# Kernel optimization log

Hardware: AMD Instinct MI355X
Metric: run time of the kernel (lower is better)

## Reference

```python
import jax, jax.numpy as jnp
import numpy as np

B = 256
NO_A, NF_A = 64, 4   # class A: n_obj, n_field (all state fields)
NO_B, NF_B = 32, 3   # class B
NS = NF_A + NF_B     # total state fields = 7
DIN, DL, DG, DH = 128, 64, 64, 256
DGE = DG * NF_A + DG * NF_B          # 448 global encoding dim
DIN_A = DGE + DL * NF_A              # 704 decoder input dim, class A
DIN_B = DGE + DL * NF_B              # 640 decoder input dim, class B
NP = 2  # distribution params per field (mean, scale)


def lrelu(x):
    return jnp.where(x >= 0, x, 0.01 * x)


def setup_inputs() -> dict:
    key = jax.random.key(0)
    ks = iter(jax.random.split(key, 40))
    def rn(shape, s=1.0):
        return jax.random.normal(next(ks), shape, jnp.float32) * s
    def w(shape):
        return rn(shape, 0.05)
    def rb(shape):
        return jax.random.randint(next(ks), shape, 0, 2).astype(bool)
    inp = dict(
        x_A=rn((B, NO_A, NF_A, DIN)),
        x_B=rn((B, NO_B, NF_B, DIN)),
        global_mask=rb((B, NS, NF_A + NF_B)),
        local_mask_A=rb((B, NF_A, NF_A)),
        local_mask_B=rb((B, NF_B, NF_B)),
        objmask_A=rb((B, NO_A)),
        objmask_B=rb((B, NO_B)),
        enc_Wl_A=w((DIN, DL)), enc_bl_A=w((DL,)),
        enc_Wg_A=w((DIN, DG)), enc_bg_A=w((DG,)),
        enc_Wl_B=w((DIN, DL)), enc_bl_B=w((DL,)),
        enc_Wg_B=w((DIN, DG)), enc_bg_B=w((DG,)),
        dec_W1_A=w((NF_A, DIN_A, DH)), dec_b1_A=w((NF_A, DH)),
        dec_W2_A=w((NF_A, DH, DH)), dec_b2_A=w((NF_A, DH)),
        dec_Wp_A=w((NF_A, DH, NP)), dec_bp_A=w((NF_A, NP)),
        dec_W1_B=w((NF_B, DIN_B, DH)), dec_b1_B=w((NF_B, DH)),
        dec_W2_B=w((NF_B, DH, DH)), dec_b2_B=w((NF_B, DH)),
        dec_Wp_B=w((NF_B, DH, NP)), dec_bp_B=w((NF_B, NP)),
        rw_W1=w((DGE, DH)), rw_b1=w((DH,)),
        rw_W2=w((DH, DH)), rw_b2=w((DH,)),
        rw_W3=w((DH, 1)), rw_b3=w((1,)),
    )
    return inp


def encode_local(x, Wl, bl, attrmask):
    # x: (B, O, F, DIN) -> (B, O, S, F*DL), masked_retain over attrmask (B, S, F)
    h = jax.nn.relu(x @ Wl + bl)                                  # (B,O,F,DL)
    y = jnp.where(attrmask[:, None, :, :, None], h[:, :, None, :, :], 0.0)  # (B,O,S,F,DL)
    return y.reshape(y.shape[0], y.shape[1], y.shape[2], -1)


def encode_global(x, Wg, bg, attrmask, objmask):
    # x: (B, O, F, DIN), attrmask: (B, NS, F), objmask: (B, O)
    h = x @ Wg + bg                                               # (B,O,F,DG)
    h = jnp.where(objmask[:, :, None, None], h, 0.0)
    r = jax.nn.relu(jnp.sum(h, axis=1))                           # (B,F,DG) sum-pool over objects
    y = jnp.where(attrmask[:, :, :, None], r[:, None], 0.0)       # (B,NS,F,DG)
    y = jnp.concatenate([y, r[:, None]], axis=1)                  # (B,NS+1,F,DG)
    return y.reshape(y.shape[0], y.shape[1], -1)


def decode(x, W1, b1, W2, b2, Wp, bp):
    # x: (B, O, S, Din); per-field (s) decoders stacked on leading axis
    h = lrelu(jnp.einsum('bosi,sid->bosd', x, W1) + b1)
    h = lrelu(jnp.einsum('bosd,sde->bose', h, W2) + b2)
    return jnp.einsum('bose,sep->bosp', h, Wp) + bp               # (B,O,S,NP)


def reference(x_A, x_B, global_mask, local_mask_A, local_mask_B, objmask_A, objmask_B,
              enc_Wl_A, enc_bl_A, enc_Wg_A, enc_bg_A,
              enc_Wl_B, enc_bl_B, enc_Wg_B, enc_bg_B,
              dec_W1_A, dec_b1_A, dec_W2_A, dec_b2_A, dec_Wp_A, dec_bp_A,
              dec_W1_B, dec_b1_B, dec_W2_B, dec_b2_B, dec_Wp_B, dec_bp_B,
              rw_W1, rw_b1, rw_W2, rw_b2, rw_W3, rw_b3):
    g_A = encode_global(x_A, enc_Wg_A, enc_bg_A, global_mask[:, :, :NF_A], objmask_A)
    g_B = encode_global(x_B, enc_Wg_B, enc_bg_B, global_mask[:, :, NF_A:], objmask_B)
    G = jnp.concatenate([g_A, g_B], axis=2)                       # (B, NS+1, DGE)

    l_A = encode_local(x_A, enc_Wl_A, enc_bl_A, local_mask_A)     # (B,NO_A,NF_A,NF_A*DL)
    gs_A = jnp.broadcast_to(G[:, None, :NF_A, :], (B, NO_A, NF_A, DGE))
    out_A = decode(jnp.concatenate([l_A, gs_A], axis=3),
                   dec_W1_A, dec_b1_A, dec_W2_A, dec_b2_A, dec_Wp_A, dec_bp_A)

    l_B = encode_local(x_B, enc_Wl_B, enc_bl_B, local_mask_B)
    gs_B = jnp.broadcast_to(G[:, None, NF_A:NS, :], (B, NO_B, NF_B, DGE))
    out_B = decode(jnp.concatenate([l_B, gs_B], axis=3),
                   dec_W1_B, dec_b1_B, dec_W2_B, dec_b2_B, dec_Wp_B, dec_bp_B)

    h = lrelu(G[:, -1, :] @ rw_W1 + rw_b1)
    h = lrelu(h @ rw_W2 + rw_b2)
    reward = (h @ rw_W3 + rw_b3)[:, 0]                            # (B,)
    return out_A, out_B, reward
```

## Files before the change

### kernel.cpp

```cpp
#include <hip/hip_runtime.h>
#include <hip/hip_bf16.h>

constexpr int Bn   = 256;
constexpr int NOA  = 64, NFA = 4;
constexpr int NOB  = 32, NFB = 3;
constexpr int NS   = 7;
constexpr int DIN  = 128, DL = 64, DG = 64, DH = 256;
constexpr int DGE  = 448;
constexpr int DINA = 704;
constexpr int DINB = 640;

typedef short  short8v __attribute__((ext_vector_type(8)));
typedef float  f32x4   __attribute__((ext_vector_type(4)));

__device__ __forceinline__ unsigned short f2bf(float x) {
  union { float f; unsigned int u; } a; a.f = x;
  unsigned int r = a.u + 0x7fff + ((a.u >> 16) & 1);
  return (unsigned short)(r >> 16);
}


struct MidArgs {
  const float *xA, *xB, *WlA, *WlB, *blA, *blB;
  unsigned short *hlA, *hlB;
  const int *omA, *omB;
  const float *WgA, *bgA, *WgB, *bgB;
  float *rA, *rB;
  const float *W1A, *W1B, *W2A, *W2B;
  unsigned short *W1tA, *W1tB, *W1gtA, *W1gtB, *W2tA, *W2tB;
};

template<int F>
__device__ void hl_body(const float* __restrict__ x, const float* __restrict__ Wl,
                        const float* __restrict__ bl, unsigned short* __restrict__ hlf,
                        int m0, unsigned char* smem) {
  auto Asb = reinterpret_cast<unsigned short(*)[72]>(smem);
  auto Bsb = reinterpret_cast<unsigned short(*)[136]>(smem + 36864);
  float (*tile)[65] = reinterpret_cast<float(*)[65]>(smem);
  const int t = threadIdx.x, w = t >> 6, lane = t & 63;
  const int lr = lane & 15, lg = lane >> 4;
  constexpr int KB1 = 2 * F;

#pragma unroll
  for (int i = 0; i < 32; ++i) {
    int idx = t + i * 256;
    tile[idx >> 6][idx & 63] = Wl[idx];
  }
  __syncthreads();
#pragma unroll
  for (int i = 0; i < 32; ++i) {
    int idx = t + i * 256;
    int n = idx >> 7, k = idx & 127;
    Bsb[n][k] = f2bf(tile[k][n]);
  }
  __syncthreads();

  f32x4 acc[4][4] = {};
  for (int k0 = 0; k0 < DIN; k0 += 64) {
    const float* xp = x + (size_t)(m0 + t) * DIN + k0;
#pragma unroll
    for (int j = 0; j < 8; ++j) {
      float4 a = *(const float4*)(xp + j * 8);
      float4 b = *(const float4*)(xp + j * 8 + 4);
      union { short8v v; unsigned short e[8]; } u;
      u.e[0] = f2bf(a.x); u.e[1] = f2bf(a.y); u.e[2] = f2bf(a.z); u.e[3] = f2bf(a.w);
      u.e[4] = f2bf(b.x); u.e[5] = f2bf(b.y); u.e[6] = f2bf(b.z); u.e[7] = f2bf(b.w);
      *reinterpret_cast<short8v*>(&Asb[t][j * 8]) = u.v;
    }
#pragma unroll
    for (int ks = 0; ks < 2; ++ks) {
      short8v af[4], bf[4];
#pragma unroll
      for (int mi = 0; mi < 4; ++mi)
        af[mi] = *reinterpret_cast<const short8v*>(&Asb[w * 64 + mi * 16 + lr][ks * 32 + lg * 8]);
#pragma unroll
      for (int ni = 0; ni < 4; ++ni)
        bf[ni] = *reinterpret_cast<const short8v*>(&Bsb[ni * 16 + lr][k0 + ks * 32 + lg * 8]);
#pragma unroll
      for (int mi = 0; mi < 4; ++mi)
#pragma unroll
        for (int ni = 0; ni < 4; ++ni)
          acc[mi][ni] = __builtin_amdgcn_mfma_f32_16x16x32_bf16(
              af[mi], bf[ni], acc[mi][ni], 0, 0, 0);
    }
  }
#pragma unroll
  for (int mi = 0; mi < 4; ++mi)
#pragma unroll
    for (int ni = 0; ni < 4; ++ni)
#pragma unroll
      for (int reg = 0; reg < 4; ++reg) {
        int row = mi * 16 + lg * 4 + reg;
        int col = ni * 16 + lr;
        float v = fmaxf(acc[mi][ni][reg] + bl[col], 0.f);
        Asb[w * 64 + row][col] = f2bf(v);
      }
  const int mpb = m0 + w * 64;
#pragma unroll
  for (int j = 0; j < 8; ++j) {
    int c = lane + j * 64;
    int ml = c >> 3, dls = c & 7;
    int mp = mpb + ml;
    int mrow = mp / F, f = mp % F;
    int m6 = mrow >> 6, mi = (mrow >> 4) & 3, lr2 = mrow & 15;
    int kb = 2 * f + (dls >> 2), lg2 = dls & 3;
    size_t dst = ((((size_t)m6 * KB1 + kb) * 4 + mi) * 64 + (lg2 * 16 + lr2)) * 8;
    *reinterpret_cast<short8v*>(hlf + dst) =
        *reinterpret_cast<const short8v*>(&Asb[w * 64 + ml][dls * 8]);
  }
}

template<int O, int F>
__device__ void xsum_rg_body(const float* __restrict__ x, const int* __restrict__ om,
                             const float* __restrict__ Wg, const float* __restrict__ bg,
                             float* __restrict__ r, int b, unsigned char* smem) {
  float* xsm = reinterpret_cast<float*>(smem + 36864 + 17408);
  const int t = threadIdx.x, f = t >> 6, lane = t & 63;
  if (f >= F) return;
  unsigned long long bal = __ballot(lane < O && om[(size_t)b * O + lane] != 0);
  float cnt = (float)__popcll(bal);
  float a0 = 0.f, a1 = 0.f;
  const float* xb = x + ((size_t)b * O * F + f) * DIN + lane;
#pragma unroll 8
  for (int o = 0; o < O; ++o) {
    float m = (float)((bal >> o) & 1ull);
    a0 += m * xb[(size_t)o * F * DIN];
    a1 += m * xb[(size_t)o * F * DIN + 64];
  }
  xsm[f * 128 + lane] = a0;
  xsm[f * 128 + lane + 64] = a1;
  asm volatile("s_waitcnt lgkmcnt(0)" ::: "memory");
  float acc = 0.f;
  const float* wp = Wg + lane;
#pragma unroll 8
  for (int i = 0; i < DIN; ++i) acc += xsm[f * 128 + i] * wp[(size_t)i * DG];
  acc += cnt * bg[lane];
  r[((size_t)b * F + f) * DG + lane] = fmaxf(acc, 0.f);
}

__device__ void wtrans_tile(const float* __restrict__ src, unsigned short* __restrict__ dst,
                            int N, int DINc, int koff, int Kout,
                            int s, int kt, int nt, unsigned char* smem) {
  float (*tile)[65] = reinterpret_cast<float(*)[65]>(smem);
  const int t = threadIdx.x;
#pragma unroll
  for (int i = 0; i < 16; ++i) {
    int rr = (t >> 6) + i * 4, c = t & 63;
    tile[rr][c] = src[((size_t)s * DINc + koff + kt * 64 + rr) * N + nt * 64 + c];
  }
  __syncthreads();
#pragma unroll
  for (int i = 0; i < 2; ++i) {
    int cidx = t + i * 256;
    int n = cidx >> 3, kc = (cidx & 7) * 8;
    union { short8v v; unsigned short e[8]; } u;
#pragma unroll
    for (int j = 0; j < 8; ++j) u.e[j] = f2bf(tile[kc + j][n]);
    *reinterpret_cast<short8v*>(dst + ((size_t)s * N + nt * 64 + n) * Kout + kt * 64 + kc) = u.v;
  }
}

__device__ void wtrans_frag(const float* __restrict__ src, unsigned short* __restrict__ dst,
                            int DINc, int koff, int KB,
                            int s, int kt, int nt, unsigned char* smem) {
  float (*tile)[65] = reinterpret_cast<float(*)[65]>(smem);
  const int t = threadIdx.x;
#pragma unroll
  for (int i = 0; i < 16; ++i) {
    int rr = (t >> 6) + i * 4, c = t & 63;
    tile[rr][c] = src[((size_t)s * DINc + koff + kt * 64 + rr) * 256 + nt * 64 + c];
  }
  __syncthreads();
#pragma unroll
  for (int i = 0; i < 2; ++i) {
    int cidx = t + i * 256;
    int nl = cidx >> 3, kslot = cidx & 7;
    union { short8v v; unsigned short e[8]; } u;
#pragma unroll
    for (int j = 0; j < 8; ++j) u.e[j] = f2bf(tile[kslot * 8 + j][nl]);
    int kb = kt * 2 + (kslot >> 2);
    int lane = (kslot & 3) * 16 + (nl & 15);
    int nchunk = nt * 4 + (nl >> 4);
    *reinterpret_cast<short8v*>(
        dst + ((((size_t)s * KB + kb) * 16 + nchunk) * 64 + lane) * 8) = u.v;
  }
}

__global__ __launch_bounds__(256) void mid_kernel(MidArgs a) {
  __shared__ __align__(16) unsigned char smem[56320];
  const int bid = blockIdx.x;
  if (bid < 256) {
    hl_body<NFA>(a.xA, a.WlA, a.blA, a.hlA, bid * 256, smem);
    xsum_rg_body<NOA, NFA>(a.xA, a.omA, a.WgA, a.bgA, a.rA, bid, smem);
  } else if (bid < 352) {
    hl_body<NFB>(a.xB, a.WlB, a.blB, a.hlB, (bid - 256) * 256, smem);
  } else if (bid < 608) {
    xsum_rg_body<NOB, NFB>(a.xB, a.omB, a.WgB, a.bgB, a.rB, bid - 352, smem);
  } else {
    int r = bid - 608;
    if (r < 64)       { wtrans_frag(a.W1A, a.W1tA, DINA, 0, 8,
                                    r / 16, (r % 16) >> 2, r & 3, smem); }
    else if (r < 100) { r -= 64;  wtrans_frag(a.W1B, a.W1tB, DINB, 0, 6,
                                    r / 12, (r % 12) >> 2, r & 3, smem); }
    else if (r < 212) { r -= 100; wtrans_tile(a.W1A, a.W1gtA, 256, DINA, NFA * DL, DGE,
                                    r / 28, (r % 28) >> 2, r & 3, smem); }
    else if (r < 296) { r -= 212; wtrans_tile(a.W1B, a.W1gtB, 256, DINB, NFB * DL, DGE,
                                    r / 28, (r % 28) >> 2, r & 3, smem); }
    else if (r < 360) { r -= 296; wtrans_frag(a.W2A, a.W2tA, DH, 0, 8,
                                    r / 16, (r % 16) >> 2, r & 3, smem); }
    else              { r -= 360; wtrans_frag(a.W2B, a.W2tB, DH, 0, 8,
                                    r / 16, (r % 16) >> 2, r & 3, smem); }
  }
}

struct GprArgs {
  const float *rA, *rB; const int *gm;
  const unsigned short *W1gtA, *W1gtB;
  const float *b1A, *b1B;
  float *g1A, *g1B;
  const float *rwW1, *rwb1, *rwW2, *rwb2, *rwW3, *rwb3;
  float *outR;
  const unsigned short *hlA, *hlB;
};

__device__ void warm_body(const unsigned short* __restrict__ p, int n16) {
  const int4* q = reinterpret_cast<const int4*>(p);
  const int t = threadIdx.x;
  for (int i = 0; i < n16; ++i) {
    int4 v = q[t + i * 256];
    asm volatile("" :: "v"(v.x), "v"(v.y), "v"(v.z), "v"(v.w));
  }
}

__device__ void gpart_body(const GprArgs& a, int bx, int sg, unsigned char* smem) {
  auto Asb = reinterpret_cast<unsigned short(*)[72]>(smem);
  auto Bsb = reinterpret_cast<unsigned short(*)[72]>(smem + 9216);
  const int t = threadIdx.x, w = t >> 6, lane = t & 63;
  const int lr = lane & 15, lg = lane >> 4;
  const int m0 = bx * 64;
  const unsigned short* W1gt; const float* b1; float* g1; int S, sl;
  if (sg < NFA) { W1gt = a.W1gtA; b1 = a.b1A; g1 = a.g1A; S = NFA; sl = sg; }
  else          { W1gt = a.W1gtB; b1 = a.b1B; g1 = a.g1B; S = NFB; sl = sg - NFA; }

  f32x4 acc[4][4] = {};
  for (int kt = 0; kt < 7; ++kt) {
    __syncthreads();
    const int f = kt;
    const float* rsrc = (f < NFA) ? (a.rA + (size_t)f * DG) : (a.rB + (size_t)(f - NFA) * DG);
    const int rstride = (f < NFA) ? NFA * DG : NFB * DG;
#pragma unroll
    for (int i = 0; i < 2; ++i) {
      int c = t + i * 256;
      int row = c >> 3, kc = (c & 7) * 8;
      int b = m0 + row;
      float mk = (a.gm[((size_t)b * NS + sg) * NS + f] != 0) ? 1.f : 0.f;
      const float* rp = rsrc + (size_t)b * rstride + kc;
      union { short8v v; unsigned short e[8]; } u;
#pragma unroll
      for (int j = 0; j < 8; ++j) u.e[j] = f2bf(mk * rp[j]);
      *reinterpret_cast<short8v*>(&Asb[row][kc]) = u.v;
    }
#pragma unroll
    for (int i = 0; i < 8; ++i) {
      int c = t + i * 256;
      int n = c >> 3, kc = (c & 7) * 8;
      *reinterpret_cast<short8v*>(&Bsb[n][kc]) = *reinterpret_cast<const short8v*>(
          W1gt + ((size_t)sl * 256 + n) * DGE + kt * 64 + kc);
    }
    __syncthreads();
#pragma unroll
    for (int ks = 0; ks < 2; ++ks) {
      short8v af[4], bf[4];
#pragma unroll
      for (int mi = 0; mi < 4; ++mi)
        af[mi] = *reinterpret_cast<const short8v*>(&Asb[mi * 16 + lr][ks * 32 + lg * 8]);
#pragma unroll
      for (int ni = 0; ni < 4; ++ni)
        bf[ni] = *reinterpret_cast<const short8v*>(&Bsb[w * 64 + ni * 16 + lr][ks * 32 + lg * 8]);
#pragma unroll
      for (int mi = 0; mi < 4; ++mi)
#pragma unroll
        for (int ni = 0; ni < 4; ++ni)
          acc[mi][ni] = __builtin_amdgcn_mfma_f32_16x16x32_bf16(
              af[mi], bf[ni], acc[mi][ni], 0, 0, 0);
    }
  }
#pragma unroll
  for (int mi = 0; mi < 4; ++mi)
#pragma unroll
    for (int reg = 0; reg < 4; ++reg) {
      int b = m0 + mi * 16 + lg * 4 + reg;
#pragma unroll
      for (int ni = 0; ni < 4; ++ni) {
        int col = w * 64 + ni * 16 + lr;
        g1[((size_t)b * S + sl) * DH + col] = acc[mi][ni][reg] + b1[(size_t)sl * DH + col];
      }
    }
}

__device__ void reward_body(const GprArgs& a, int b, unsigned char* smem) {
  float* Gs = reinterpret_cast<float*>(smem);
  float* h1 = Gs + DGE;
  float* red = h1 + DH;
  const int t = threadIdx.x;
  for (int j = t; j < DGE; j += 256)
    Gs[j] = (j < NFA * DG) ? a.rA[((size_t)b * NFA + (j >> 6)) * DG + (j & 63)]
                           : a.rB[((size_t)b * NFB + ((j - NFA * DG) >> 6)) * DG + (j & 63)];
  __syncthreads();
  float acc = a.rwb1[t];
  for (int j = 0; j < DGE; ++j) acc += Gs[j] * a.rwW1[(size_t)j * DH + t];
  h1[t] = (acc >= 0.f) ? acc : 0.01f * acc;
  __syncthreads();
  acc = a.rwb2[t];
  for (int j = 0; j < DH; ++j) acc += h1[j] * a.rwW2[(size_t)j * DH + t];
  acc = (acc >= 0.f) ? acc : 0.01f * acc;
  red[t] = acc * a.rwW3[t];
  __syncthreads();
  for (int off = 128; off > 0; off >>= 1) {
    if (t < off) red[t] += red[t + off];
    __syncthreads();
  }
  if (t == 0) a.outR[b] = red[0] + a.rwb3[0];
}

__global__ __launch_bounds__(256) void gpr_kernel(GprArgs a) {
  __shared__ __align__(16) unsigned char smem[46080];
  const int bid = blockIdx.x;
  if (bid < 256) {
    int xcd = bid & 7, idx = bid >> 3;
    int m6 = (idx >> 1) * 16 + xcd * 2 + (idx & 1);
    warm_body(a.hlA + (size_t)m6 * 16384, 8);
  } else if (bid < 384) {
    int local = bid - 256;
    int xcd = local & 7, idx = local >> 3;
    int m6 = (idx >> 1) * 16 + xcd * 2 + (idx & 1);
    warm_body(a.hlB + (size_t)m6 * 12288, 6);
  } else if (bid < 412) {
    gpart_body(a, (bid - 384) & 3, (bid - 384) >> 2, smem);
  } else {
    reward_body(a, bid - 412, smem);
  }
}

struct DecArgs {
  const unsigned short *hlA, *hlB, *W1tA, *W1tB, *W2tA, *W2tB;
  const int *lmA, *lmB;
  const float *g1A, *g1B, *WpA, *WpB, *b2A, *b2B, *bpA, *bpB;
  float *outA, *outB;
};

template<int NO, int F>
__device__ __forceinline__ void dec_body(
    int mt, int s, unsigned short* h1s , float* red ,
    const unsigned short* __restrict__ hlf, const int* __restrict__ lm,
    const float* __restrict__ g1,
    const unsigned short* __restrict__ W1f, const unsigned short* __restrict__ W2f,
    const float* __restrict__ Wp, const float* __restrict__ b2,
    const float* __restrict__ bp, float* __restrict__ out) {
  constexpr int KB1 = 2 * F;
  const int t = threadIdx.x, w = t >> 6, lane = t & 63;
  const int lr = lane & 15, lg = lane >> 4;
  const int mh = w >> 2, nq = w & 3;
  const int m6 = mt * 2 + mh;
  const int m0 = mt * 128;

  unsigned mkl = 0, mkh = 0;
#pragma unroll
  for (int f = 0; f < F; ++f) {
    if (NO == 64) {
      unsigned bit = (lm[((size_t)m6 * F + s) * F + f] != 0) ? 1u : 0u;
      mkl |= bit << f; mkh |= bit << f;
    } else {
      int b0 = m6 * 2;
      if (lm[((size_t)b0 * F + s) * F + f])       mkl |= 1u << f;
      if (lm[((size_t)(b0 + 1) * F + s) * F + f]) mkh |= 1u << f;
    }
  }
  float g1r[2][4];
#pragma unroll
  for (int ni = 0; ni < 4; ++ni) {
    int col = nq * 64 + ni * 16 + lr;
    if (NO == 64) {
      g1r[0][ni] = g1[((size_t)m6 * F + s) * DH + col];
      g1r[1][ni] = g1r[0][ni];
    } else {
      g1r[0][ni] = g1[((size_t)(m6 * 2) * F + s) * DH + col];
      g1r[1][ni] = g1[((size_t)(m6 * 2 + 1) * F + s) * DH + col];
    }
  }

  f32x4 acc[4][4] = {};
  const short8v zero8 = {0, 0, 0, 0, 0, 0, 0, 0};

  const unsigned short* Afb = hlf + (size_t)m6 * KB1 * 2048 + lane * 8;
  const unsigned short* B1b = W1f + ((size_t)s * KB1 * 16 + nq * 4) * 512 + lane * 8;
#pragma unroll
  for (int kb = 0; kb < KB1; ++kb) {
    const int f = kb >> 1;
    short8v af[4], bf[4];
#pragma unroll
    for (int mi = 0; mi < 4; ++mi)
      af[mi] = *reinterpret_cast<const short8v*>(Afb + (size_t)kb * 2048 + mi * 512);
    const bool bl = (mkl >> f) & 1, bh = (mkh >> f) & 1;
#pragma unroll
    for (int mi = 0; mi < 4; ++mi) {
      const bool ok = (mi < 2) ? bl : bh;
      af[mi] = ok ? af[mi] : zero8;
    }
#pragma unroll
    for (int ni = 0; ni < 4; ++ni)
      bf[ni] = *reinterpret_cast<const short8v*>(B1b + (size_t)kb * 8192 + ni * 512);
#pragma unroll
    for (int mi = 0; mi < 4; ++mi)
#pragma unroll
      for (int ni = 0; ni < 4; ++ni)
        acc[mi][ni] = __builtin_amdgcn_mfma_f32_16x16x32_bf16(
            af[mi], bf[ni], acc[mi][ni], 0, 0, 0);
  }

#pragma unroll
  for (int mi = 0; mi < 4; ++mi) {
    int gi = (NO == 32) ? (mi >> 1) : 0;
#pragma unroll
    for (int reg = 0; reg < 4; ++reg) {
      int row = mh * 64 + mi * 16 + lg * 4 + reg;
#pragma unroll
      for (int ni = 0; ni < 4; ++ni) {
        int col = nq * 64 + ni * 16 + lr;
        float v = acc[mi][ni][reg] + g1r[gi][ni];
        v = (v >= 0.f) ? v : 0.01f * v;
        h1s[row * 264 + col] = f2bf(v);
        acc[mi][ni][reg] = 0.f;
      }
    }
  }
  __syncthreads();

  const unsigned short* B2b = W2f + ((size_t)s * 8 * 16 + nq * 4) * 512 + lane * 8;
#pragma unroll
  for (int kb = 0; kb < 8; ++kb) {
    short8v af[4], bf[4];
#pragma unroll
    for (int mi = 0; mi < 4; ++mi)
      af[mi] = *reinterpret_cast<const short8v*>(
          h1s + (mh * 64 + mi * 16 + lr) * 264 + kb * 32 + lg * 8);
#pragma unroll
    for (int ni = 0; ni < 4; ++ni)
      bf[ni] = *reinterpret_cast<const short8v*>(B2b + (size_t)kb * 8192 + ni * 512);
#pragma unroll
    for (int mi = 0; mi < 4; ++mi)
#pragma unroll
      for (int ni = 0; ni < 4; ++ni)
        acc[mi][ni] = __builtin_amdgcn_mfma_f32_16x16x32_bf16(
            af[mi], bf[ni], acc[mi][ni], 0, 0, 0);
  }

  float part[4][4][2] = {};
  const float* Wps = Wp + (size_t)s * DH * 2;
  const float* b2s = b2 + (size_t)s * DH;
#pragma unroll
  for (int ni = 0; ni < 4; ++ni) {
    int col = nq * 64 + ni * 16 + lr;
    float wp0 = Wps[col * 2 + 0], wp1 = Wps[col * 2 + 1], bb2 = b2s[col];
#pragma unroll
    for (int mi = 0; mi < 4; ++mi)
#pragma unroll
      for (int reg = 0; reg < 4; ++reg) {
        float v = acc[mi][ni][reg] + bb2;
        v = (v >= 0.f) ? v : 0.01f * v;
        part[mi][reg][0] += v * wp0;
        part[mi][reg][1] += v * wp1;
      }
  }
#pragma unroll
  for (int off = 1; off < 16; off <<= 1)
#pragma unroll
    for (int mi = 0; mi < 4; ++mi)
#pragma unroll
      for (int reg = 0; reg < 4; ++reg) {
        part[mi][reg][0] += __shfl_xor(part[mi][reg][0], off, 64);
        part[mi][reg][1] += __shfl_xor(part[mi][reg][1], off, 64);
      }
  if (lr == 0)
#pragma unroll
    for (int mi = 0; mi < 4; ++mi)
#pragma unroll
      for (int reg = 0; reg < 4; ++reg) {
        int rowin = mi * 16 + lg * 4 + reg;
        red[((size_t)w * 64 + rowin) * 2 + 0] = part[mi][reg][0];
        red[((size_t)w * 64 + rowin) * 2 + 1] = part[mi][reg][1];
      }
  __syncthreads();
  if (t < 256) {
    int row = t >> 1, p = t & 1;
    int mhr = row >> 6, rowin = row & 63;
    float sum = 0.f;
#pragma unroll
    for (int q = 0; q < 4; ++q)
      sum += red[((size_t)(mhr * 4 + q) * 64 + rowin) * 2 + p];
    out[((size_t)(m0 + row) * F + s) * 2 + p] = sum + bp[(size_t)s * 2 + p];
  }
}

__global__ __launch_bounds__(512, 4) void dec_kernel(DecArgs a) {
  __shared__ __align__(16) unsigned short h1s[128 * 264];
  __shared__ float red[1024];
  const int bid = blockIdx.x;
  if (bid < 512) {
    dec_body<NOA, NFA>(bid & 127, bid >> 7, h1s, red, a.hlA, a.lmA, a.g1A,
                       a.W1tA, a.W2tA, a.WpA, a.b2A, a.bpA, a.outA);
  } else {
    int r = bid - 512;
    dec_body<NOB, NFB>(r & 63, r >> 6, h1s, red, a.hlB, a.lmB, a.g1B,
                       a.W1tB, a.W2tB, a.WpB, a.b2B, a.bpB, a.outB);
  }
}

extern "C" void kernel_launch(void* const* d_in, const int* in_sizes, int n_in,
                              void* d_out, int out_size, void* d_ws, size_t ws_size,
                              hipStream_t stream) {
  const float* x_A  = (const float*)d_in[0];
  const float* x_B  = (const float*)d_in[1];
  const int*   gm   = (const int*)d_in[2];
  const int*   lmA  = (const int*)d_in[3];
  const int*   lmB  = (const int*)d_in[4];
  const int*   omA  = (const int*)d_in[5];
  const int*   omB  = (const int*)d_in[6];
  const float* Wl_A = (const float*)d_in[7];
  const float* bl_A = (const float*)d_in[8];
  const float* Wg_A = (const float*)d_in[9];
  const float* bg_A = (const float*)d_in[10];
  const float* Wl_B = (const float*)d_in[11];
  const float* bl_B = (const float*)d_in[12];
  const float* Wg_B = (const float*)d_in[13];
  const float* bg_B = (const float*)d_in[14];
  const float* W1_A = (const float*)d_in[15];
  const float* b1_A = (const float*)d_in[16];
  const float* W2_A = (const float*)d_in[17];
  const float* b2_A = (const float*)d_in[18];
  const float* Wp_A = (const float*)d_in[19];
  const float* bp_A = (const float*)d_in[20];
  const float* W1_B = (const float*)d_in[21];
  const float* b1_B = (const float*)d_in[22];
  const float* W2_B = (const float*)d_in[23];
  const float* b2_B = (const float*)d_in[24];
  const float* Wp_B = (const float*)d_in[25];
  const float* bp_B = (const float*)d_in[26];
  const float* rwW1 = (const float*)d_in[27];
  const float* rwb1 = (const float*)d_in[28];
  const float* rwW2 = (const float*)d_in[29];
  const float* rwb2 = (const float*)d_in[30];
  const float* rwW3 = (const float*)d_in[31];
  const float* rwb3 = (const float*)d_in[32];

  float* ws   = (float*)d_ws;
  float* rA   = ws;
  float* rB   = rA + 65536;
  float* g1A  = rB + 49152;
  float* g1B  = g1A + 262144;
  unsigned short* us    = (unsigned short*)(g1B + 196608);
  unsigned short* hlA   = us;
  unsigned short* hlB   = hlA + 4194304;
  unsigned short* W1tA  = hlB + 1572864;
  unsigned short* W1tB  = W1tA + 262144;
  unsigned short* W2tA  = W1tB + 147456;
  unsigned short* W2tB  = W2tA + 262144;
  unsigned short* W1gtA = W2tB + 196608;
  unsigned short* W1gtB = W1gtA + 458752;

  float* outA = (float*)d_out;
  float* outB = outA + 131072;
  float* outR = outA + 180224;

  MidArgs m;
  m.xA = x_A; m.xB = x_B; m.WlA = Wl_A; m.WlB = Wl_B; m.blA = bl_A; m.blB = bl_B;
  m.hlA = hlA; m.hlB = hlB; m.omA = omA; m.omB = omB;
  m.WgA = Wg_A; m.bgA = bg_A; m.WgB = Wg_B; m.bgB = bg_B;
  m.rA = rA; m.rB = rB;
  m.W1A = W1_A; m.W1B = W1_B; m.W2A = W2_A; m.W2B = W2_B;
  m.W1tA = W1tA; m.W1tB = W1tB; m.W1gtA = W1gtA; m.W1gtB = W1gtB;
  m.W2tA = W2tA; m.W2tB = W2tB;

  GprArgs g;
  g.rA = rA; g.rB = rB; g.gm = gm; g.W1gtA = W1gtA; g.W1gtB = W1gtB;
  g.b1A = b1_A; g.b1B = b1_B; g.g1A = g1A; g.g1B = g1B;
  g.rwW1 = rwW1; g.rwb1 = rwb1; g.rwW2 = rwW2; g.rwb2 = rwb2;
  g.rwW3 = rwW3; g.rwb3 = rwb3; g.outR = outR;
  g.hlA = hlA; g.hlB = hlB;

  DecArgs d;
  d.hlA = hlA; d.hlB = hlB; d.W1tA = W1tA; d.W1tB = W1tB;
  d.W2tA = W2tA; d.W2tB = W2tB; d.lmA = lmA; d.lmB = lmB;
  d.g1A = g1A; d.g1B = g1B; d.WpA = Wp_A; d.WpB = Wp_B;
  d.b2A = b2_A; d.b2B = b2_B; d.bpA = bp_A; d.bpB = bp_B;
  d.outA = outA; d.outB = outB;

  mid_kernel<<<1016, 256, 0, stream>>>(m);
  gpr_kernel<<<668, 256, 0, stream>>>(g);
  dec_kernel<<<704, 512, 0, stream>>>(d);
}
```

Before: 94.42 us.

## Fuse local encoder into decoder kernel, keeping hl activations in LDS

The local-encoder GEMM (x @ Wl, relu) now runs inside the decoder kernel. Each block computes its 64-row hl tile straight into shared memory and loops over all state fields s, instead of writing hl to global memory and reading it back. The cache-warming blocks and the global hl buffer are removed, and Wl is pre-packed into MFMA fragment layout in the first kernel. The trade-off is fewer, larger decoder blocks: 384 blocks of 256 threads replace 704 of 512, each doing F sequential passes, which lowers parallelism and occupancy.

```diff
diff --git a/kernel.cpp b/kernel.cpp
--- a/kernel.cpp
+++ b/kernel.cpp
@@ -20,101 +20,20 @@
 }
 
 
-struct MidArgs {
-  const float *xA, *xB, *WlA, *WlB, *blA, *blB;
-  unsigned short *hlA, *hlB;
+struct Pre1Args {
+  const float *xA, *xB;
   const int *omA, *omB;
   const float *WgA, *bgA, *WgB, *bgB;
   float *rA, *rB;
-  const float *W1A, *W1B, *W2A, *W2B;
-  unsigned short *W1tA, *W1tB, *W1gtA, *W1gtB, *W2tA, *W2tB;
+  const float *WlA, *WlB, *W1A, *W1B, *W2A, *W2B;
+  unsigned short *WlFA, *WlFB, *W1tA, *W1tB, *W1gtA, *W1gtB, *W2tA, *W2tB;
 };
-
-template<int F>
-__device__ void hl_body(const float* __restrict__ x, const float* __restrict__ Wl,
-                        const float* __restrict__ bl, unsigned short* __restrict__ hlf,
-                        int m0, unsigned char* smem) {
-  auto Asb = reinterpret_cast<unsigned short(*)[72]>(smem);
-  auto Bsb = reinterpret_cast<unsigned short(*)[136]>(smem + 36864);
-  float (*tile)[65] = reinterpret_cast<float(*)[65]>(smem);
-  const int t = threadIdx.x, w = t >> 6, lane = t & 63;
-  const int lr = lane & 15, lg = lane >> 4;
-  constexpr int KB1 = 2 * F;
-
-#pragma unroll
-  for (int i = 0; i < 32; ++i) {
-    int idx = t + i * 256;
-    tile[idx >> 6][idx & 63] = Wl[idx];
-  }
-  __syncthreads();
-#pragma unroll
-  for (int i = 0; i < 32; ++i) {
-    int idx = t + i * 256;
-    int n = idx >> 7, k = idx & 127;
-    Bsb[n][k] = f2bf(tile[k][n]);
-  }
-  __syncthreads();
-
-  f32x4 acc[4][4] = {};
-  for (int k0 = 0; k0 < DIN; k0 += 64) {
-    const float* xp = x + (size_t)(m0 + t) * DIN + k0;
-#pragma unroll
-    for (int j = 0; j < 8; ++j) {
-      float4 a = *(const float4*)(xp + j * 8);
-      float4 b = *(const float4*)(xp + j * 8 + 4);
-      union { short8v v; unsigned short e[8]; } u;
-      u.e[0] = f2bf(a.x); u.e[1] = f2bf(a.y); u.e[2] = f2bf(a.z); u.e[3] = f2bf(a.w);
-      u.e[4] = f2bf(b.x); u.e[5] = f2bf(b.y); u.e[6] = f2bf(b.z); u.e[7] = f2bf(b.w);
-      *reinterpret_cast<short8v*>(&Asb[t][j * 8]) = u.v;
-    }
-#pragma unroll
-    for (int ks = 0; ks < 2; ++ks) {
-      short8v af[4], bf[4];
-#pragma unroll
-      for (int mi = 0; mi < 4; ++mi)
-        af[mi] = *reinterpret_cast<const short8v*>(&Asb[w * 64 + mi * 16 + lr][ks * 32 + lg * 8]);
-#pragma unroll
-      for (int ni = 0; ni < 4; ++ni)
-        bf[ni] = *reinterpret_cast<const short8v*>(&Bsb[ni * 16 + lr][k0 + ks * 32 + lg * 8]);
-#pragma unroll
-      for (int mi = 0; mi < 4; ++mi)
-#pragma unroll
-        for (int ni = 0; ni < 4; ++ni)
-          acc[mi][ni] = __builtin_amdgcn_mfma_f32_16x16x32_bf16(
-              af[mi], bf[ni], acc[mi][ni], 0, 0, 0);
-    }
-  }
-#pragma unroll
-  for (int mi = 0; mi < 4; ++mi)
-#pragma unroll
-    for (int ni = 0; ni < 4; ++ni)
-#pragma unroll
-      for (int reg = 0; reg < 4; ++reg) {
-        int row = mi * 16 + lg * 4 + reg;
-        int col = ni * 16 + lr;
-        float v = fmaxf(acc[mi][ni][reg] + bl[col], 0.f);
-        Asb[w * 64 + row][col] = f2bf(v);
-      }
-  const int mpb = m0 + w * 64;
-#pragma unroll
-  for (int j = 0; j < 8; ++j) {
-    int c = lane + j * 64;
-    int ml = c >> 3, dls = c & 7;
-    int mp = mpb + ml;
-    int mrow = mp / F, f = mp % F;
-    int m6 = mrow >> 6, mi = (mrow >> 4) & 3, lr2 = mrow & 15;
-    int kb = 2 * f + (dls >> 2), lg2 = dls & 3;
-    size_t dst = ((((size_t)m6 * KB1 + kb) * 4 + mi) * 64 + (lg2 * 16 + lr2)) * 8;
-    *reinterpret_cast<short8v*>(hlf + dst) =
-        *reinterpret_cast<const short8v*>(&Asb[w * 64 + ml][dls * 8]);
-  }
-}
 
 template<int O, int F>
 __device__ void xsum_rg_body(const float* __restrict__ x, const int* __restrict__ om,
                              const float* __restrict__ Wg, const float* __restrict__ bg,
-                             float* __restrict__ r, int b, unsigned char* smem) {
-  float* xsm = reinterpret_cast<float*>(smem + 36864 + 17408);
+                             float* __restrict__ r, int b, float* smem) {
+  float* xsm = smem;
   const int t = threadIdx.x, f = t >> 6, lane = t & 63;
   if (f >= F) return;
   unsigned long long bal = __ballot(lane < O && om[(size_t)b * O + lane] != 0);
@@ -140,7 +59,7 @@
 
 __device__ void wtrans_tile(const float* __restrict__ src, unsigned short* __restrict__ dst,
                             int N, int DINc, int koff, int Kout,
-                            int s, int kt, int nt, unsigned char* smem) {
+                            int s, int kt, int nt, float* smem) {
   float (*tile)[65] = reinterpret_cast<float(*)[65]>(smem);
   const int t = threadIdx.x;
 #pragma unroll
@@ -162,7 +81,7 @@
 
 __device__ void wtrans_frag(const float* __restrict__ src, unsigned short* __restrict__ dst,
                             int DINc, int koff, int KB,
-                            int s, int kt, int nt, unsigned char* smem) {
+                            int s, int kt, int nt, float* smem) {
   float (*tile)[65] = reinterpret_cast<float(*)[65]>(smem);
   const int t = threadIdx.x;
 #pragma unroll
@@ -186,53 +105,66 @@
   }
 }
 
-__global__ __launch_bounds__(256) void mid_kernel(MidArgs a) {
-  __shared__ __align__(16) unsigned char smem[56320];
+__device__ void wl_frag(const float* __restrict__ src, unsigned short* __restrict__ dst,
+                        int kt, float* smem) {
+  float (*tile)[65] = reinterpret_cast<float(*)[65]>(smem);
+  const int t = threadIdx.x;
+#pragma unroll
+  for (int i = 0; i < 16; ++i) {
+    int rr = (t >> 6) + i * 4, c = t & 63;
+    tile[rr][c] = src[(size_t)(kt * 64 + rr) * 64 + c];
+  }
+  __syncthreads();
+#pragma unroll
+  for (int i = 0; i < 2; ++i) {
+    int cidx = t + i * 256;
+    int nl = cidx >> 3, kslot = cidx & 7;
+    union { short8v v; unsigned short e[8]; } u;
+#pragma unroll
+    for (int j = 0; j < 8; ++j) u.e[j] = f2bf(tile[kslot * 8 + j][nl]);
+    int kb = kt * 2 + (kslot >> 2);
+    int lane = (kslot & 3) * 16 + (nl & 15);
+    int nchunk = nl >> 4;
+    *reinterpret_cast<short8v*>(dst + (((size_t)kb * 4 + nchunk) * 64 + lane) * 8) = u.v;
+  }
+}
+
+__global__ __launch_bounds__(256) void pre1_kernel(Pre1Args a) {
+  __shared__ __align__(16) float smem[64 * 65];
   const int bid = blockIdx.x;
   if (bid < 256) {
-    hl_body<NFA>(a.xA, a.WlA, a.blA, a.hlA, bid * 256, smem);
     xsum_rg_body<NOA, NFA>(a.xA, a.omA, a.WgA, a.bgA, a.rA, bid, smem);
-  } else if (bid < 352) {
-    hl_body<NFB>(a.xB, a.WlB, a.blB, a.hlB, (bid - 256) * 256, smem);
-  } else if (bid < 608) {
-    xsum_rg_body<NOB, NFB>(a.xB, a.omB, a.WgB, a.bgB, a.rB, bid - 352, smem);
+  } else if (bid < 512) {
+    xsum_rg_body<NOB, NFB>(a.xB, a.omB, a.WgB, a.bgB, a.rB, bid - 256, smem);
   } else {
-    int r = bid - 608;
-    if (r < 64)       { wtrans_frag(a.W1A, a.W1tA, DINA, 0, 8,
+    int r = bid - 512;
+    if (r < 2)        wl_frag(a.WlA, a.WlFA, r, smem);
+    else if (r < 4)   wl_frag(a.WlB, a.WlFB, r - 2, smem);
+    else if (r < 68)  { r -= 4;   wtrans_frag(a.W1A, a.W1tA, DINA, 0, 8,
                                     r / 16, (r % 16) >> 2, r & 3, smem); }
-    else if (r < 100) { r -= 64;  wtrans_frag(a.W1B, a.W1tB, DINB, 0, 6,
+    else if (r < 104) { r -= 68;  wtrans_frag(a.W1B, a.W1tB, DINB, 0, 6,
                                     r / 12, (r % 12) >> 2, r & 3, smem); }
-    else if (r < 212) { r -= 100; wtrans_tile(a.W1A, a.W1gtA, 256, DINA, NFA * DL, DGE,
+    else if (r < 216) { r -= 104; wtrans_tile(a.W1A, a.W1gtA, 256, DINA, NFA * DL, DGE,
                                     r / 28, (r % 28) >> 2, r & 3, smem); }
-    else if (r < 296) { r -= 212; wtrans_tile(a.W1B, a.W1gtB, 256, DINB, NFB * DL, DGE,
+    else if (r < 300) { r -= 216; wtrans_tile(a.W1B, a.W1gtB, 256, DINB, NFB * DL, DGE,
                                     r / 28, (r % 28) >> 2, r & 3, smem); }
-    else if (r < 360) { r -= 296; wtrans_frag(a.W2A, a.W2tA, DH, 0, 8,
+    else if (r < 364) { r -= 300; wtrans_frag(a.W2A, a.W2tA, DH, 0, 8,
                                     r / 16, (r % 16) >> 2, r & 3, smem); }
-    else              { r -= 360; wtrans_frag(a.W2B, a.W2tB, DH, 0, 8,
+    else              { r -= 364; wtrans_frag(a.W2B, a.W2tB, DH, 0, 8,
                                     r / 16, (r % 16) >> 2, r & 3, smem); }
   }
 }
 
-struct GprArgs {
+struct Pre2Args {
   const float *rA, *rB; const int *gm;
   const unsigned short *W1gtA, *W1gtB;
   const float *b1A, *b1B;
   float *g1A, *g1B;
   const float *rwW1, *rwb1, *rwW2, *rwb2, *rwW3, *rwb3;
   float *outR;
-  const unsigned short *hlA, *hlB;
 };
 
-__device__ void warm_body(const unsigned short* __restrict__ p, int n16) {
-  const int4* q = reinterpret_cast<const int4*>(p);
-  const int t = threadIdx.x;
-  for (int i = 0; i < n16; ++i) {
-    int4 v = q[t + i * 256];
-    asm volatile("" :: "v"(v.x), "v"(v.y), "v"(v.z), "v"(v.w));
-  }
-}
-
-__device__ void gpart_body(const GprArgs& a, int bx, int sg, unsigned char* smem) {
+__device__ void gpart_body(const Pre2Args& a, int bx, int sg, unsigned char* smem) {
   auto Asb = reinterpret_cast<unsigned short(*)[72]>(smem);
   auto Bsb = reinterpret_cast<unsigned short(*)[72]>(smem + 9216);
   const int t = threadIdx.x, w = t >> 6, lane = t & 63;
@@ -298,7 +230,7 @@
     }
 }
 
-__device__ void reward_body(const GprArgs& a, int b, unsigned char* smem) {
+__device__ void reward_body(const Pre2Args& a, int b, unsigned char* smem) {
   float* Gs = reinterpret_cast<float*>(smem);
   float* h1 = Gs + DGE;
   float* red = h1 + DH;
@@ -323,196 +255,264 @@
   if (t == 0) a.outR[b] = red[0] + a.rwb3[0];
 }
 
-__global__ __launch_bounds__(256) void gpr_kernel(GprArgs a) {
+__global__ __launch_bounds__(256) void pre2_kernel(Pre2Args a) {
   __shared__ __align__(16) unsigned char smem[46080];
   const int bid = blockIdx.x;
-  if (bid < 256) {
-    int xcd = bid & 7, idx = bid >> 3;
-    int m6 = (idx >> 1) * 16 + xcd * 2 + (idx & 1);
-    warm_body(a.hlA + (size_t)m6 * 16384, 8);
-  } else if (bid < 384) {
-    int local = bid - 256;
-    int xcd = local & 7, idx = local >> 3;
-    int m6 = (idx >> 1) * 16 + xcd * 2 + (idx & 1);
-    warm_body(a.hlB + (size_t)m6 * 12288, 6);
-  } else if (bid < 412) {
-    gpart_body(a, (bid - 384) & 3, (bid - 384) >> 2, smem);
-  } else {
-    reward_body(a, bid - 412, smem);
-  }
-}
-
-struct DecArgs {
-  const unsigned short *hlA, *hlB, *W1tA, *W1tB, *W2tA, *W2tB;
+  if (bid < 28) gpart_body(a, bid & 3, bid >> 2, smem);
+  else          reward_body(a, bid - 28, smem);
+}
+
+struct FusedArgs {
+  const float *xA, *xB;
+  const unsigned short *WlFA, *WlFB;
+  const float *blA, *blB;
+  const unsigned short *W1tA, *W1tB, *W2tA, *W2tB;
   const int *lmA, *lmB;
   const float *g1A, *g1B, *WpA, *WpB, *b2A, *b2B, *bpA, *bpB;
   float *outA, *outB;
 };
 
 template<int NO, int F>
-__device__ __forceinline__ void dec_body(
-    int mt, int s, unsigned short* h1s , float* red ,
-    const unsigned short* __restrict__ hlf, const int* __restrict__ lm,
-    const float* __restrict__ g1,
+__device__ __forceinline__ void fused_body(
+    int blk,
+    unsigned short* hl_lds , unsigned short* scratch ,
+    float* red ,
+    const float* __restrict__ x, const unsigned short* __restrict__ WlF,
+    const float* __restrict__ bl,
     const unsigned short* __restrict__ W1f, const unsigned short* __restrict__ W2f,
+    const int* __restrict__ lm, const float* __restrict__ g1,
     const float* __restrict__ Wp, const float* __restrict__ b2,
     const float* __restrict__ bp, float* __restrict__ out) {
   constexpr int KB1 = 2 * F;
   const int t = threadIdx.x, w = t >> 6, lane = t & 63;
   const int lr = lane & 15, lg = lane >> 4;
-  const int mh = w >> 2, nq = w & 3;
-  const int m6 = mt * 2 + mh;
-  const int m0 = mt * 128;
-
-  unsigned mkl = 0, mkh = 0;
-#pragma unroll
-  for (int f = 0; f < F; ++f) {
-    if (NO == 64) {
-      unsigned bit = (lm[((size_t)m6 * F + s) * F + f] != 0) ? 1u : 0u;
-      mkl |= bit << f; mkh |= bit << f;
+  const int m0 = blk * 64;
+
+  short8v bfwl[4][4];
+#pragma unroll
+  for (int kb = 0; kb < 4; ++kb)
+#pragma unroll
+    for (int ni = 0; ni < 4; ++ni)
+      bfwl[kb][ni] = *reinterpret_cast<const short8v*>(
+          WlF + (((size_t)kb * 4 + ni) * 64 + lane) * 8);
+
+  f32x4 acc[4][4] = {};
+  auto Asb = reinterpret_cast<unsigned short(*)[72]>(scratch);
+
+  {
+    const float* xp_base = x + ((size_t)m0 * F + t) * DIN;
+    for (int k0 = 0; k0 < DIN; k0 += 64) {
+      if (t < 64 * F) {
+        const float* xp = xp_base + k0;
+#pragma unroll
+        for (int j = 0; j < 8; ++j) {
+          float4 va = *(const float4*)(xp + j * 8);
+          float4 vb = *(const float4*)(xp + j * 8 + 4);
+          union { short8v v; unsigned short e[8]; } u;
+          u.e[0] = f2bf(va.x); u.e[1] = f2bf(va.y); u.e[2] = f2bf(va.z); u.e[3] = f2bf(va.w);
+          u.e[4] = f2bf(vb.x); u.e[5] = f2bf(vb.y); u.e[6] = f2bf(vb.z); u.e[7] = f2bf(vb.w);
+          *reinterpret_cast<short8v*>(&Asb[t][j * 8]) = u.v;
+        }
+      }
+      if (w < F) {
+#pragma unroll
+        for (int ks = 0; ks < 2; ++ks) {
+          int kb = (k0 >> 5) + ks;
+          short8v af[4];
+#pragma unroll
+          for (int mi = 0; mi < 4; ++mi)
+            af[mi] = *reinterpret_cast<const short8v*>(
+                &Asb[w * 64 + mi * 16 + lr][ks * 32 + lg * 8]);
+#pragma unroll
+          for (int mi = 0; mi < 4; ++mi)
+#pragma unroll
+            for (int ni = 0; ni < 4; ++ni)
+              acc[mi][ni] = __builtin_amdgcn_mfma_f32_16x16x32_bf16(
+                  af[mi], bfwl[kb][ni], acc[mi][ni], 0, 0, 0);
+        }
+      }
+    }
+    __syncthreads();
+    if (w < F) {
+#pragma unroll
+      for (int mi = 0; mi < 4; ++mi)
+#pragma unroll
+        for (int reg = 0; reg < 4; ++reg) {
+          int mp = w * 64 + mi * 16 + lg * 4 + reg;
+          int row = mp / F, f = mp - row * F;
+#pragma unroll
+          for (int ni = 0; ni < 4; ++ni) {
+            int dl = ni * 16 + lr;
+            float v = fmaxf(acc[mi][ni][reg] + bl[dl], 0.f);
+            hl_lds[row * 264 + f * 64 + dl] = f2bf(v);
+            acc[mi][ni][reg] = 0.f;
+          }
+        }
     } else {
-      int b0 = m6 * 2;
-      if (lm[((size_t)b0 * F + s) * F + f])       mkl |= 1u << f;
-      if (lm[((size_t)(b0 + 1) * F + s) * F + f]) mkh |= 1u << f;
-    }
-  }
-  float g1r[2][4];
-#pragma unroll
-  for (int ni = 0; ni < 4; ++ni) {
-    int col = nq * 64 + ni * 16 + lr;
-    if (NO == 64) {
-      g1r[0][ni] = g1[((size_t)m6 * F + s) * DH + col];
-      g1r[1][ni] = g1r[0][ni];
-    } else {
-      g1r[0][ni] = g1[((size_t)(m6 * 2) * F + s) * DH + col];
-      g1r[1][ni] = g1[((size_t)(m6 * 2 + 1) * F + s) * DH + col];
-    }
-  }
-
-  f32x4 acc[4][4] = {};
+#pragma unroll
+      for (int mi = 0; mi < 4; ++mi)
+#pragma unroll
+        for (int ni = 0; ni < 4; ++ni)
+#pragma unroll
+          for (int reg = 0; reg < 4; ++reg) acc[mi][ni][reg] = 0.f;
+    }
+    __syncthreads();
+  }
+
+  unsigned short* h1s = scratch;
   const short8v zero8 = {0, 0, 0, 0, 0, 0, 0, 0};
 
-  const unsigned short* Afb = hlf + (size_t)m6 * KB1 * 2048 + lane * 8;
-  const unsigned short* B1b = W1f + ((size_t)s * KB1 * 16 + nq * 4) * 512 + lane * 8;
-#pragma unroll
-  for (int kb = 0; kb < KB1; ++kb) {
-    const int f = kb >> 1;
-    short8v af[4], bf[4];
-#pragma unroll
-    for (int mi = 0; mi < 4; ++mi)
-      af[mi] = *reinterpret_cast<const short8v*>(Afb + (size_t)kb * 2048 + mi * 512);
-    const bool bl = (mkl >> f) & 1, bh = (mkh >> f) & 1;
+  for (int s = 0; s < F; ++s) {
+    unsigned mkl = 0, mkh = 0;
+#pragma unroll
+    for (int f = 0; f < F; ++f) {
+      if (NO == 64) {
+        unsigned bit = (lm[((size_t)blk * F + s) * F + f] != 0) ? 1u : 0u;
+        mkl |= bit << f; mkh |= bit << f;
+      } else {
+        int b0 = blk * 2;
+        if (lm[((size_t)b0 * F + s) * F + f])       mkl |= 1u << f;
+        if (lm[((size_t)(b0 + 1) * F + s) * F + f]) mkh |= 1u << f;
+      }
+    }
+    float g1v[2][4];
+#pragma unroll
+    for (int ni = 0; ni < 4; ++ni) {
+      int col = w * 64 + ni * 16 + lr;
+      if (NO == 64) {
+        g1v[0][ni] = g1[((size_t)blk * F + s) * DH + col];
+        g1v[1][ni] = g1v[0][ni];
+      } else {
+        g1v[0][ni] = g1[((size_t)(blk * 2) * F + s) * DH + col];
+        g1v[1][ni] = g1[((size_t)(blk * 2 + 1) * F + s) * DH + col];
+      }
+    }
+
+#pragma unroll
+    for (int kb = 0; kb < KB1; ++kb) {
+      const int f = kb >> 1;
+      short8v af[4], bf[4];
+#pragma unroll
+      for (int mi = 0; mi < 4; ++mi)
+        af[mi] = *reinterpret_cast<const short8v*>(
+            hl_lds + (mi * 16 + lr) * 264 + kb * 32 + lg * 8);
+      const bool blo = (mkl >> f) & 1, bhi = (mkh >> f) & 1;
+#pragma unroll
+      for (int mi = 0; mi < 4; ++mi) {
+        const bool ok = (mi < 2) ? blo : bhi;
+        af[mi] = ok ? af[mi] : zero8;
+      }
+      const unsigned short* bb =
+          W1f + (((size_t)s * KB1 + kb) * 16 + w * 4) * 512 + lane * 8;
+#pragma unroll
+      for (int ni = 0; ni < 4; ++ni)
+        bf[ni] = *reinterpret_cast<const short8v*>(bb + ni * 512);
+#pragma unroll
+      for (int mi = 0; mi < 4; ++mi)
+#pragma unroll
+        for (int ni = 0; ni < 4; ++ni)
+          acc[mi][ni] = __builtin_amdgcn_mfma_f32_16x16x32_bf16(
+              af[mi], bf[ni], acc[mi][ni], 0, 0, 0);
+    }
+
 #pragma unroll
     for (int mi = 0; mi < 4; ++mi) {
-      const bool ok = (mi < 2) ? bl : bh;
-      af[mi] = ok ? af[mi] : zero8;
-    }
-#pragma unroll
-    for (int ni = 0; ni < 4; ++ni)
-      bf[ni] = *reinterpret_cast<const short8v*>(B1b + (size_t)kb * 8192 + ni * 512);
-#pragma unroll
-    for (int mi = 0; mi < 4; ++mi)
+      int gi = (NO == 32) ? (mi >> 1) : 0;
+#pragma unroll
+      for (int reg = 0; reg < 4; ++reg) {
+        int row = mi * 16 + lg * 4 + reg;
+#pragma unroll
+        for (int ni = 0; ni < 4; ++ni) {
+          int col = w * 64 + ni * 16 + lr;
+          float v = acc[mi][ni][reg] + g1v[gi][ni];
+          v = (v >= 0.f) ? v : 0.01f * v;
+          h1s[row * 264 + col] = f2bf(v);
+          acc[mi][ni][reg] = 0.f;
+        }
+      }
+    }
+    __syncthreads();
+
+#pragma unroll
+    for (int kb = 0; kb < 8; ++kb) {
+      short8v af[4], bf[4];
+#pragma unroll
+      for (int mi = 0; mi < 4; ++mi)
+        af[mi] = *reinterpret_cast<const short8v*>(
+            h1s + (mi * 16 + lr) * 264 + kb * 32 + lg * 8);
+      const unsigned short* bb =
+          W2f + (((size_t)s * 8 + kb) * 16 + w * 4) * 512 + lane * 8;
 #pragma unroll
       for (int ni = 0; ni < 4; ++ni)
-        acc[mi][ni] = __builtin_amdgcn_mfma_f32_16x16x32_bf16(
-            af[mi], bf[ni], acc[mi][ni], 0, 0, 0);
-  }
-
-#pragma unroll
-  for (int mi = 0; mi < 4; ++mi) {
-    int gi = (NO == 32) ? (mi >> 1) : 0;
-#pragma unroll
-    for (int reg = 0; reg < 4; ++reg) {
-      int row = mh * 64 + mi * 16 + lg * 4 + reg;
-#pragma unroll
-      for (int ni = 0; ni < 4; ++ni) {
-        int col = nq * 64 + ni * 16 + lr;
-        float v = acc[mi][ni][reg] + g1r[gi][ni];
-        v = (v >= 0.f) ? v : 0.01f * v;
-        h1s[row * 264 + col] = f2bf(v);
-        acc[mi][ni][reg] = 0.f;
-      }
-    }
-  }
-  __syncthreads();
-
-  const unsigned short* B2b = W2f + ((size_t)s * 8 * 16 + nq * 4) * 512 + lane * 8;
-#pragma unroll
-  for (int kb = 0; kb < 8; ++kb) {
-    short8v af[4], bf[4];
-#pragma unroll
-    for (int mi = 0; mi < 4; ++mi)
-      af[mi] = *reinterpret_cast<const short8v*>(
-          h1s + (mh * 64 + mi * 16 + lr) * 264 + kb * 32 + lg * 8);
-#pragma unroll
-    for (int ni = 0; ni < 4; ++ni)
-      bf[ni] = *reinterpret_cast<const short8v*>(B2b + (size_t)kb * 8192 + ni * 512);
-#pragma unroll
-    for (int mi = 0; mi < 4; ++mi)
-#pragma unroll
-      for (int ni = 0; ni < 4; ++ni)
-        acc[mi][ni] = __builtin_amdgcn_mfma_f32_16x16x32_bf16(
-            af[mi], bf[ni], acc[mi][ni], 0, 0, 0);
-  }
-
-  float part[4][4][2] = {};
-  const float* Wps = Wp + (size_t)s * DH * 2;
-  const float* b2s = b2 + (size_t)s * DH;
-#pragma unroll
-  for (int ni = 0; ni < 4; ++ni) {
-    int col = nq * 64 + ni * 16 + lr;
-    float wp0 = Wps[col * 2 + 0], wp1 = Wps[col * 2 + 1], bb2 = b2s[col];
-#pragma unroll
-    for (int mi = 0; mi < 4; ++mi)
-#pragma unroll
-      for (int reg = 0; reg < 4; ++reg) {
-        float v = acc[mi][ni][reg] + bb2;
-        v = (v >= 0.f) ? v : 0.01f * v;
-        part[mi][reg][0] += v * wp0;
-        part[mi][reg][1] += v * wp1;
-      }
-  }
-#pragma unroll
-  for (int off = 1; off < 16; off <<= 1)
-#pragma unroll
-    for (int mi = 0; mi < 4; ++mi)
-#pragma unroll
-      for (int reg = 0; reg < 4; ++reg) {
-        part[mi][reg][0] += __shfl_xor(part[mi][reg][0], off, 64);
-        part[mi][reg][1] += __shfl_xor(part[mi][reg][1], off, 64);
-      }
-  if (lr == 0)
-#pragma unroll
-    for (int mi = 0; mi < 4; ++mi)
-#pragma unroll
-      for (int reg = 0; reg < 4; ++reg) {
-        int rowin = mi * 16 + lg * 4 + reg;
-        red[((size_t)w * 64 + rowin) * 2 + 0] = part[mi][reg][0];
-        red[((size_t)w * 64 + rowin) * 2 + 1] = part[mi][reg][1];
-      }
-  __syncthreads();
-  if (t < 256) {
-    int row = t >> 1, p = t & 1;
-    int mhr = row >> 6, rowin = row & 63;
-    float sum = 0.f;
-#pragma unroll
-    for (int q = 0; q < 4; ++q)
-      sum += red[((size_t)(mhr * 4 + q) * 64 + rowin) * 2 + p];
-    out[((size_t)(m0 + row) * F + s) * 2 + p] = sum + bp[(size_t)s * 2 + p];
-  }
-}
-
-__global__ __launch_bounds__(512, 4) void dec_kernel(DecArgs a) {
-  __shared__ __align__(16) unsigned short h1s[128 * 264];
-  __shared__ float red[1024];
+        bf[ni] = *reinterpret_cast<const short8v*>(bb + ni * 512);
+#pragma unroll
+      for (int mi = 0; mi < 4; ++mi)
+#pragma unroll
+        for (int ni = 0; ni < 4; ++ni)
+          acc[mi][ni] = __builtin_amdgcn_mfma_f32_16x16x32_bf16(
+              af[mi], bf[ni], acc[mi][ni], 0, 0, 0);
+    }
+
+    float part[4][4][2] = {};
+    const float* Wps = Wp + (size_t)s * DH * 2;
+    const float* b2s = b2 + (size_t)s * DH;
+#pragma unroll
+    for (int ni = 0; ni < 4; ++ni) {
+      int col = w * 64 + ni * 16 + lr;
+      float wp0 = Wps[col * 2 + 0], wp1 = Wps[col * 2 + 1], bb2 = b2s[col];
+#pragma unroll
+      for (int mi = 0; mi < 4; ++mi)
+#pragma unroll
+        for (int reg = 0; reg < 4; ++reg) {
+          float v = acc[mi][ni][reg] + bb2;
+          v = (v >= 0.f) ? v : 0.01f * v;
+          part[mi][reg][0] += v * wp0;
+          part[mi][reg][1] += v * wp1;
+          acc[mi][ni][reg] = 0.f;
+        }
+    }
+#pragma unroll
+    for (int off = 1; off < 16; off <<= 1)
+#pragma unroll
+      for (int mi = 0; mi < 4; ++mi)
+#pragma unroll
+        for (int reg = 0; reg < 4; ++reg) {
+          part[mi][reg][0] += __shfl_xor(part[mi][reg][0], off, 64);
+          part[mi][reg][1] += __shfl_xor(part[mi][reg][1], off, 64);
+        }
+    if (lr == 0)
+#pragma unroll
+      for (int mi = 0; mi < 4; ++mi)
+#pragma unroll
+        for (int reg = 0; reg < 4; ++reg) {
+          int row = mi * 16 + lg * 4 + reg;
+          red[((size_t)w * 64 + row) * 2 + 0] = part[mi][reg][0];
+          red[((size_t)w * 64 + row) * 2 + 1] = part[mi][reg][1];
+        }
+    __syncthreads();
+    if (t < 128) {
+      int row = t >> 1, p = t & 1;
+      float sum = red[(0 * 64 + row) * 2 + p] + red[(1 * 64 + row) * 2 + p]
+                + red[(2 * 64 + row) * 2 + p] + red[(3 * 64 + row) * 2 + p];
+      out[((size_t)(m0 + row) * F + s) * 2 + p] = sum + bp[(size_t)s * 2 + p];
+    }
+    __syncthreads();
+  }
+}
+
+__global__ __launch_bounds__(256) void fused_kernel(FusedArgs a) {
+  __shared__ __align__(16) unsigned short hl_lds[64 * 264];
+  __shared__ __align__(16) unsigned short scratch[256 * 72];
+  __shared__ __align__(16) float red[512];
   const int bid = blockIdx.x;
-  if (bid < 512) {
-    dec_body<NOA, NFA>(bid & 127, bid >> 7, h1s, red, a.hlA, a.lmA, a.g1A,
-                       a.W1tA, a.W2tA, a.WpA, a.b2A, a.bpA, a.outA);
+  if (bid < 256) {
+    fused_body<NOA, NFA>(bid, hl_lds, scratch, red,
+                         a.xA, a.WlFA, a.blA, a.W1tA, a.W2tA,
+                         a.lmA, a.g1A, a.WpA, a.b2A, a.bpA, a.outA);
   } else {
-    int r = bid - 512;
-    dec_body<NOB, NFB>(r & 63, r >> 6, h1s, red, a.hlB, a.lmB, a.g1B,
-                       a.W1tB, a.W2tB, a.WpB, a.b2B, a.bpB, a.outB);
+    fused_body<NOB, NFB>(bid - 256, hl_lds, scratch, red,
+                         a.xB, a.WlFB, a.blB, a.W1tB, a.W2tB,
+                         a.lmB, a.g1B, a.WpB, a.b2B, a.bpB, a.outB);
   }
 }
 
@@ -559,43 +559,43 @@
   float* g1A  = rB + 49152;
   float* g1B  = g1A + 262144;
   unsigned short* us    = (unsigned short*)(g1B + 196608);
-  unsigned short* hlA   = us;
-  unsigned short* hlB   = hlA + 4194304;
-  unsigned short* W1tA  = hlB + 1572864;
+  unsigned short* W1tA  = us;
   unsigned short* W1tB  = W1tA + 262144;
   unsigned short* W2tA  = W1tB + 147456;
   unsigned short* W2tB  = W2tA + 262144;
   unsigned short* W1gtA = W2tB + 196608;
   unsigned short* W1gtB = W1gtA + 458752;
+  unsigned short* WlFA  = W1gtB + 344064;
+  unsigned short* WlFB  = WlFA + 8192;
 
   float* outA = (float*)d_out;
   float* outB = outA + 131072;
   float* outR = outA + 180224;
 
-  MidArgs m;
-  m.xA = x_A; m.xB = x_B; m.WlA = Wl_A; m.WlB = Wl_B; m.blA = bl_A; m.blB = bl_B;
-  m.hlA = hlA; m.hlB = hlB; m.omA = omA; m.omB = omB;
-  m.WgA = Wg_A; m.bgA = bg_A; m.WgB = Wg_B; m.bgB = bg_B;
-  m.rA = rA; m.rB = rB;
-  m.W1A = W1_A; m.W1B = W1_B; m.W2A = W2_A; m.W2B = W2_B;
-  m.W1tA = W1tA; m.W1tB = W1tB; m.W1gtA = W1gtA; m.W1gtB = W1gtB;
-  m.W2tA = W2tA; m.W2tB = W2tB;
-
-  GprArgs g;
-  g.rA = rA; g.rB = rB; g.gm = gm; g.W1gtA = W1gtA; g.W1gtB = W1gtB;
-  g.b1A = b1_A; g.b1B = b1_B; g.g1A = g1A; g.g1B = g1B;
-  g.rwW1 = rwW1; g.rwb1 = rwb1; g.rwW2 = rwW2; g.rwb2 = rwb2;
-  g.rwW3 = rwW3; g.rwb3 = rwb3; g.outR = outR;
-  g.hlA = hlA; g.hlB = hlB;
-
-  DecArgs d;
-  d.hlA = hlA; d.hlB = hlB; d.W1tA = W1tA; d.W1tB = W1tB;
-  d.W2tA = W2tA; d.W2tB = W2tB; d.lmA = lmA; d.lmB = lmB;
-  d.g1A = g1A; d.g1B = g1B; d.WpA = Wp_A; d.WpB = Wp_B;
-  d.b2A = b2_A; d.b2B = b2_B; d.bpA = bp_A; d.bpB = bp_B;
-  d.outA = outA; d.outB = outB;
-
-  mid_kernel<<<1016, 256, 0, stream>>>(m);
-  gpr_kernel<<<668, 256, 0, stream>>>(g);
-  dec_kernel<<<704, 512, 0, stream>>>(d);
-}
+  Pre1Args p1;
+  p1.xA = x_A; p1.xB = x_B; p1.omA = omA; p1.omB = omB;
+  p1.WgA = Wg_A; p1.bgA = bg_A; p1.WgB = Wg_B; p1.bgB = bg_B;
+  p1.rA = rA; p1.rB = rB;
+  p1.WlA = Wl_A; p1.WlB = Wl_B; p1.W1A = W1_A; p1.W1B = W1_B;
+  p1.W2A = W2_A; p1.W2B = W2_B;
+  p1.WlFA = WlFA; p1.WlFB = WlFB; p1.W1tA = W1tA; p1.W1tB = W1tB;
+  p1.W1gtA = W1gtA; p1.W1gtB = W1gtB; p1.W2tA = W2tA; p1.W2tB = W2tB;
+
+  Pre2Args p2;
+  p2.rA = rA; p2.rB = rB; p2.gm = gm; p2.W1gtA = W1gtA; p2.W1gtB = W1gtB;
+  p2.b1A = b1_A; p2.b1B = b1_B; p2.g1A = g1A; p2.g1B = g1B;
+  p2.rwW1 = rwW1; p2.rwb1 = rwb1; p2.rwW2 = rwW2; p2.rwb2 = rwb2;
+  p2.rwW3 = rwW3; p2.rwb3 = rwb3; p2.outR = outR;
+
+  FusedArgs fa;
+  fa.xA = x_A; fa.xB = x_B; fa.WlFA = WlFA; fa.WlFB = WlFB;
+  fa.blA = bl_A; fa.blB = bl_B;
+  fa.W1tA = W1tA; fa.W1tB = W1tB; fa.W2tA = W2tA; fa.W2tB = W2tB;
+  fa.lmA = lmA; fa.lmB = lmB; fa.g1A = g1A; fa.g1B = g1B;
+  fa.WpA = Wp_A; fa.WpB = Wp_B; fa.b2A = b2_A; fa.b2B = b2_B;
+  fa.bpA = bp_A; fa.bpB = bp_B; fa.outA = outA; fa.outB = outB;
+
+  pre1_kernel<<<924, 256, 0, stream>>>(p1);
+  pre2_kernel<<<284, 256, 0, stream>>>(p2);
+  fused_kernel<<<384, 256, 0, stream>>>(fa);
+}
```

New measurement: 133.3 us. 1.41x slower.
